# Optimization experiments

Hardware: AMD Instinct MI355X
Metric: run time of the kernel (lower is better)

Reference implementation:

```python
import jax, jax.numpy as jnp
import numpy as np

N = 100000   # nodes
E = 1600000  # edges
F = 64       # num_features
H = 64       # hidden_units
C = 10       # num_classes
G = 1000     # graphs in batch
BN_EPS = 1e-5


def setup_inputs() -> dict:
    key = jax.random.key(0)
    ks = jax.random.split(key, 32)
    inp = {
        "x": jax.random.normal(ks[0], (N, F), dtype=jnp.float32),
        "edge_index": jax.random.randint(ks[1], (2, E), 0, N, dtype=jnp.int64),
        "batch": jnp.sort(jax.random.randint(ks[2], (N,), 0, G, dtype=jnp.int64)),
    }
    i = 3
    def w(shape, scale):
        nonlocal i
        a = jax.random.normal(ks[i], shape, dtype=jnp.float32) * scale
        i += 1
        return a
    for l, din in [(0, F), (1, H)]:
        inp[f"c{l}_w1"] = w((din, H), 1.0 / np.sqrt(din))
        inp[f"c{l}_b1"] = jnp.zeros((H,), jnp.float32)
        inp[f"c{l}_g1"] = jnp.ones((H,), jnp.float32)
        inp[f"c{l}_be1"] = jnp.zeros((H,), jnp.float32)
        inp[f"c{l}_w2"] = w((H, H), 1.0 / np.sqrt(H))
        inp[f"c{l}_b2"] = jnp.zeros((H,), jnp.float32)
        inp[f"bn{l}_g"] = jnp.ones((H,), jnp.float32)
        inp[f"bn{l}_b"] = jnp.zeros((H,), jnp.float32)
    for l, din in [(0, F), (1, H), (2, H)]:
        inp[f"l{l}_w"] = w((din, C), 1.0 / np.sqrt(din))
        inp[f"l{l}_b"] = jnp.zeros((C,), jnp.float32)
    return inp


def _bn(h, g, b):
    # BatchNorm1d in training mode: batch statistics over node axis
    m = jnp.mean(h, axis=0)
    v = jnp.var(h, axis=0)
    return g * (h - m) * jax.lax.rsqrt(v + BN_EPS) + b


def _gin_conv(h, src, dst, w1, b1, g1, be1, w2, b2):
    # scatter-add neighbor aggregation: out[dst] += h[src]; eps = 0
    agg = jax.ops.segment_sum(h[src], dst, num_segments=N)
    z = h + agg                      # (1 + eps) * x + sum_j x_j
    z = jax.nn.relu(_bn(z @ w1 + b1, g1, be1))
    return z @ w2 + b2


def reference(x, edge_index, batch,
              c0_w1, c0_b1, c0_g1, c0_be1, c0_w2, c0_b2, bn0_g, bn0_b,
              c1_w1, c1_b1, c1_g1, c1_be1, c1_w2, c1_b2, bn1_g, bn1_b,
              l0_w, l0_b, l1_w, l1_b, l2_w, l2_b):
    src, dst = edge_index[0], edge_index[1]
    h0 = x
    h1 = jax.nn.relu(_bn(_gin_conv(h0, src, dst, c0_w1, c0_b1, c0_g1, c0_be1, c0_w2, c0_b2), bn0_g, bn0_b))
    h2 = jax.nn.relu(_bn(_gin_conv(h1, src, dst, c1_w1, c1_b1, c1_g1, c1_be1, c1_w2, c1_b2), bn1_g, bn1_b))
    # jumping-knowledge readout: per-layer global_add_pool -> Linear -> sum (dropout=0)
    out = jnp.zeros((G, C), dtype=x.dtype)
    for h, w, b in [(h0, l0_w, l0_b), (h1, l1_w, l1_b), (h2, l2_w, l2_b)]:
        pooled = jax.ops.segment_sum(h, batch, num_segments=G)
        out = out + pooled @ w + b
    return out
```

## Files before the change

### kernel.cpp

```cpp
#include <hip/hip_runtime.h>
#include <hip/hip_bf16.h>

#define BN_EPS 1e-5f
#define NBMAX 512
#define CHUNK 4096
#define CAP   5120
#define CAPC  6144

typedef __hip_bfloat16 bf16;
typedef __attribute__((ext_vector_type(8))) short short8;
typedef __attribute__((ext_vector_type(4))) float f32x4;

__device__ __forceinline__ float b2f(bf16 v) { return __bfloat162float(v); }
__device__ __forceinline__ bf16 f2b(float v) { return __float2bfloat16(v); }
__device__ __forceinline__ float bl(unsigned u) { return __uint_as_float(u << 16); }
__device__ __forceinline__ float bh(unsigned u) { return __uint_as_float(u & 0xffff0000u); }
__device__ __forceinline__ unsigned pack2(float x, float y) {
    union { bf16 b[2]; unsigned u; } p;
    p.b[0] = f2b(x); p.b[1] = f2b(y);
    return p.u;
}
__device__ __forceinline__ float bs2f(short s) {
    return __uint_as_float(((unsigned)(unsigned short)s) << 16);
}
__device__ __forceinline__ short f2bs(float v) {
    bf16 b = f2b(v);
    return *reinterpret_cast<short*>(&b);
}

__global__ __launch_bounds__(256) void initcast_k(
    const float* __restrict__ in, bf16* __restrict__ out, int total4,
    int* __restrict__ bcur, int NB)
{
    if (blockIdx.x == 0) {
        for (int i = threadIdx.x; i < NB; i += 256) bcur[i] = i * CAP;
    }
    int i = blockIdx.x * 256 + threadIdx.x;
    if (i >= total4) return;
    float4 v = ((const float4*)in)[i];
    union { ushort4 u; bf16 b[4]; } p;
    p.b[0] = f2b(v.x); p.b[1] = f2b(v.y); p.b[2] = f2b(v.z); p.b[3] = f2b(v.w);
    ((ushort4*)out)[i] = p.u;
}

__global__ __launch_bounds__(256) void binscatter_k(
    const int* __restrict__ src, const int* __restrict__ dst,
    int* __restrict__ bcur, int* __restrict__ tmp, int E, int NB)
{
    __shared__ int hist[NBMAX];
    __shared__ int loff[NBMAX];
    __shared__ int gb[NBMAX];
    __shared__ int lcur[NBMAX];
    __shared__ int staged[CHUNK];
    __shared__ unsigned short sb[CHUNK];
    __shared__ int ssc[256];
    const int t = threadIdx.x;
    for (int i = t; i < NB; i += 256) { hist[i] = 0; lcur[i] = 0; }
    __syncthreads();
    const int base = blockIdx.x * CHUNK;
    const int lim = min(CHUNK, E - base);
    int myb[16], myw[16];
    int cnt = 0;
    for (int i = t; i < lim; i += 256) {
        int d = dst[base + i];
        int s_ = src[base + i];
        int b = d >> 8;
        myb[cnt] = b;
        myw[cnt] = (s_ << 8) | (d & 255);
        cnt++;
        atomicAdd(&hist[b], 1);
    }
    __syncthreads();
    int v0 = (2 * t     < NB) ? hist[2 * t]     : 0;
    int v1 = (2 * t + 1 < NB) ? hist[2 * t + 1] : 0;
    ssc[t] = v0 + v1;
    __syncthreads();
    for (int off = 1; off < 256; off <<= 1) {
        int a = (t >= off) ? ssc[t - off] : 0;
        __syncthreads();
        ssc[t] += a;
        __syncthreads();
    }
    int excl = ssc[t] - (v0 + v1);
    if (2 * t < NB)     loff[2 * t] = excl;
    if (2 * t + 1 < NB) loff[2 * t + 1] = excl + v0;
    __syncthreads();
    for (int b = t; b < NB; b += 256)
        if (hist[b] > 0) gb[b] = atomicAdd(&bcur[b], hist[b]);
    for (int i = 0; i < cnt; i++) {
        int b = myb[i];
        int p = loff[b] + atomicAdd(&lcur[b], 1);
        staged[p] = myw[i];
        sb[p] = (unsigned short)b;
    }
    __syncthreads();
    for (int i = t; i < lim; i += 256) {
        int b = sb[i];
        tmp[gb[b] + (i - loff[b])] = staged[i];
    }
}

__global__ __launch_bounds__(256) void csr_k(
    const int* __restrict__ bcur, const int* __restrict__ tmp,
    int* __restrict__ rowptr, int* __restrict__ rowend,
    int* __restrict__ adj, int N)
{
    __shared__ int hist[256], pfx[256], cur[256], ssc[256];
    __shared__ int sadj[CAPC];
    const int b = blockIdx.x, t = threadIdx.x;
    const int lo = b * CAP;
    const int cnt = min(bcur[b] - lo, CAP);
    hist[t] = 0; cur[t] = 0;
    __syncthreads();
    for (int i = t; i < cnt; i += 256)
        atomicAdd(&hist[tmp[lo + i] & 255], 1);
    __syncthreads();
    int v = hist[t];
    ssc[t] = v;
    __syncthreads();
    for (int off = 1; off < 256; off <<= 1) {
        int a = (t >= off) ? ssc[t - off] : 0;
        __syncthreads();
        ssc[t] += a;
        __syncthreads();
    }
    pfx[t] = ssc[t] - v;
    const int node = b * 256 + t;
    if (node < N) {
        rowptr[node] = lo + pfx[t];
        rowend[node] = lo + pfx[t] + v;
    }
    __syncthreads();
    if (cnt <= CAPC) {
        for (int i = t; i < cnt; i += 256) {
            int w = tmp[lo + i];
            int d = w & 255;
            int p = pfx[d] + atomicAdd(&cur[d], 1);
            sadj[p] = w >> 8;
        }
        __syncthreads();
        for (int i = t; i < cnt; i += 256) adj[lo + i] = sadj[i];
    } else {
        for (int i = t; i < cnt; i += 256) {
            int w = tmp[lo + i];
            int d = w & 255;
            int p = pfx[d] + atomicAdd(&cur[d], 1);
            adj[lo + p] = w >> 8;
        }
    }
}

template<int AFFINE>
__global__ __launch_bounds__(256) void aggregate_k(
    const bf16* __restrict__ h, const int* __restrict__ rowptr,
    const int* __restrict__ rowend, const int* __restrict__ adj,
    bf16* __restrict__ z, int N,
    const float* __restrict__ sc, const float* __restrict__ sh)
{
    const int lane = threadIdx.x & 31;
    const int n = blockIdx.x * 8 + (threadIdx.x >> 5);
    float sc0 = 0.f, sc1 = 0.f, sh0 = 0.f, sh1 = 0.f;
    if (AFFINE) {
        const int f0 = lane * 2;
        sc0 = sc[f0]; sc1 = sc[f0 + 1];
        sh0 = sh[f0]; sh1 = sh[f0 + 1];
    }
    if (n >= N) return;
    const unsigned* hp = (const unsigned*)h;
    const int b = rowptr[n], e = rowend[n];

    unsigned u = hp[(size_t)n * 32 + lane];
    float a0 = bl(u), a1 = bh(u);
    if (AFFINE) {
        a0 = fmaxf(fmaf(a0, sc0, sh0), 0.f);
        a1 = fmaxf(fmaf(a1, sc1, sh1), 0.f);
    }
    float s0 = a0, s1 = a1;

    int i = b;
    for (; i + 16 <= e; i += 16) {
        int m[16];
        #pragma unroll
        for (int k = 0; k < 16; k++) m[k] = adj[i + k];
        unsigned w[16];
        #pragma unroll
        for (int k = 0; k < 16; k++) w[k] = hp[(size_t)m[k] * 32 + lane];
        #pragma unroll
        for (int k = 0; k < 16; k++) {
            float p0 = bl(w[k]), p1 = bh(w[k]);
            if (AFFINE) {
                p0 = fmaxf(fmaf(p0, sc0, sh0), 0.f);
                p1 = fmaxf(fmaf(p1, sc1, sh1), 0.f);
            }
            s0 += p0; s1 += p1;
        }
    }
    for (; i + 4 <= e; i += 4) {
        int m[4];
        #pragma unroll
        for (int k = 0; k < 4; k++) m[k] = adj[i + k];
        #pragma unroll
        for (int k = 0; k < 4; k++) {
            unsigned w = hp[(size_t)m[k] * 32 + lane];
            float p0 = bl(w), p1 = bh(w);
            if (AFFINE) {
                p0 = fmaxf(fmaf(p0, sc0, sh0), 0.f);
                p1 = fmaxf(fmaf(p1, sc1, sh1), 0.f);
            }
            s0 += p0; s1 += p1;
        }
    }
    for (; i < e; i++) {
        unsigned w = hp[(size_t)adj[i] * 32 + lane];
        float p0 = bl(w), p1 = bh(w);
        if (AFFINE) {
            p0 = fmaxf(fmaf(p0, sc0, sh0), 0.f);
            p1 = fmaxf(fmaf(p1, sc1, sh1), 0.f);
        }
        s0 += p0; s1 += p1;
    }
    ((unsigned*)z)[(size_t)n * 32 + lane] = pack2(s0, s1);
}

template<int MODE>
__global__ __launch_bounds__(256) void gemm64_k(
    const bf16* __restrict__ A,
    const float* __restrict__ scin, const float* __restrict__ shin,
    const float* __restrict__ W, const float* __restrict__ bias,
    bf16* __restrict__ out, float* __restrict__ pstat, int nrows)
{
    __shared__ bf16 sWt[64][72];
    __shared__ bf16 sC[128][68];
    __shared__ float sSc[64], sSh[64], sB[64];
    __shared__ float sredS[64][17], sredQ[64][17];
    const int tid = threadIdx.x;

    if (tid < 64) {
        sB[tid] = bias[tid];
        if (MODE == 1) { sSc[tid] = scin[tid]; sSh[tid] = shin[tid]; }
    }
    for (int i = tid; i < 4096; i += 256) {
        int k = i >> 6, n = i & 63;
        sWt[n][k] = f2b(W[i]);
    }
    __syncthreads();

    const int wave = tid >> 6, lane = tid & 63;
    const int quad = lane >> 4, l16 = lane & 15;
    const int row0 = blockIdx.x * 128 + wave * 32;

    short8 a[2][2];
    #pragma unroll
    for (int rt = 0; rt < 2; rt++) {
        int r = row0 + rt * 16 + l16;
        int rr = min(r, nrows - 1);
        const bf16* arow = A + (size_t)rr * 64;
        a[rt][0] = *(const short8*)(arow + quad * 8);
        a[rt][1] = *(const short8*)(arow + 32 + quad * 8);
        if (MODE == 1) {
            #pragma unroll
            for (int j = 0; j < 8; j++) {
                int f0 = quad * 8 + j;
                a[rt][0][j] = f2bs(fmaxf(fmaf(bs2f(a[rt][0][j]), sSc[f0], sSh[f0]), 0.f));
                int f1 = 32 + f0;
                a[rt][1][j] = f2bs(fmaxf(fmaf(bs2f(a[rt][1][j]), sSc[f1], sSh[f1]), 0.f));
            }
        }
    }

    float psS[4], psQ[4];
    #pragma unroll
    for (int t = 0; t < 4; t++) { psS[t] = 0.f; psQ[t] = 0.f; }

    #pragma unroll
    for (int t = 0; t < 4; t++) {
        const int n = t * 16 + l16;
        short8 b0 = *(const short8*)&sWt[n][quad * 8];
        short8 b1 = *(const short8*)&sWt[n][32 + quad * 8];
        const float bn_ = sB[n];
        #pragma unroll
        for (int rt = 0; rt < 2; rt++) {
            f32x4 acc = {0.f, 0.f, 0.f, 0.f};
            acc = __builtin_amdgcn_mfma_f32_16x16x32_bf16(a[rt][0], b0, acc, 0, 0, 0);
            acc = __builtin_amdgcn_mfma_f32_16x16x32_bf16(a[rt][1], b1, acc, 0, 0, 0);
            #pragma unroll
            for (int reg = 0; reg < 4; reg++) {
                const int lr = wave * 32 + rt * 16 + quad * 4 + reg;
                float v = acc[reg] + bn_;
                sC[lr][n] = f2b(v);
                if (row0 + rt * 16 + quad * 4 + reg < nrows) {
                    psS[t] += v;
                    psQ[t] = fmaf(v, v, psQ[t]);
                }
            }
        }
    }

    #pragma unroll
    for (int t = 0; t < 4; t++) {
        sredS[t * 16 + l16][wave * 4 + quad] = psS[t];
        sredQ[t * 16 + l16][wave * 4 + quad] = psQ[t];
    }
    __syncthreads();

    const int gbase = blockIdx.x * 128;
    #pragma unroll
    for (int it = 0; it < 8; it++) {
        int idx = it * 256 + tid;
        int r = idx >> 4, c4 = idx & 15;
        if (gbase + r < nrows) {
            ushort4 v = *(const ushort4*)&sC[r][c4 * 4];
            *(ushort4*)(out + (size_t)(gbase + r) * 64 + c4 * 4) = v;
        }
    }

    if (tid < 128) {
        const int c = tid & 63;
        const float* p = (tid < 64) ? &sredS[c][0] : &sredQ[c][0];
        float s = 0.f;
        #pragma unroll
        for (int i = 0; i < 16; i++) s += p[i];
        pstat[(size_t)blockIdx.x * 128 + (tid < 64 ? c : 64 + c)] = s;
    }
}

__global__ __launch_bounds__(256) void bn_reduce_k(
    const float* __restrict__ pstat, int nblk,
    const float* __restrict__ g, const float* __restrict__ be, float invN,
    float* __restrict__ sc, float* __restrict__ sh)
{
    const int f = blockIdx.x;
    const int t = threadIdx.x;
    float S = 0.f, Q = 0.f;
    for (int b = t; b < nblk; b += 256) {
        S += pstat[(size_t)b * 128 + f];
        Q += pstat[(size_t)b * 128 + 64 + f];
    }
    __shared__ float rs[256], rq[256];
    rs[t] = S; rq[t] = Q;
    __syncthreads();
    for (int off = 128; off > 0; off >>= 1) {
        if (t < off) { rs[t] += rs[t + off]; rq[t] += rq[t + off]; }
        __syncthreads();
    }
    if (t == 0) {
        float m = rs[0] * invN;
        float v = rq[0] * invN - m * m;
        float s = g[f] * rsqrtf(v + BN_EPS);
        sc[f] = s;
        sh[f] = be[f] - m * s;
    }
}

__global__ __launch_bounds__(256) void pool_readout_k(
    const bf16* __restrict__ xb, const bf16* __restrict__ z0,
    const bf16* __restrict__ z1, const int* __restrict__ batch,
    const float* __restrict__ scA, const float* __restrict__ shA,
    const float* __restrict__ scB, const float* __restrict__ shB,
    const float* __restrict__ w0, const float* __restrict__ b0,
    const float* __restrict__ w1, const float* __restrict__ b1,
    const float* __restrict__ w2, const float* __restrict__ b2,
    float* __restrict__ out, int Nn)
{
    const int g = blockIdx.x;
    int lo = 0, hi = Nn;
    while (lo < hi) { int mid = (lo + hi) >> 1; if (batch[mid] < g) lo = mid + 1; else hi = mid; }
    const int start = lo;
    hi = Nn;
    while (lo < hi) { int mid = (lo + hi) >> 1; if (batch[mid] <= g) lo = mid + 1; else hi = mid; }
    const int end = lo;

    const int f = threadIdx.x & 63;
    const int w = threadIdx.x >> 6;
    const float sA = scA[f], tA = shA[f];
    const float sB = scB[f], tB = shB[f];

    float s0 = 0.f, s1 = 0.f, s2 = 0.f;
    for (int i = start + w; i < end; i += 4) {
        s0 += b2f(xb[(size_t)i * 64 + f]);
        s1 += fmaxf(fmaf(b2f(z0[(size_t)i * 64 + f]), sA, tA), 0.f);
        s2 += fmaxf(fmaf(b2f(z1[(size_t)i * 64 + f]), sB, tB), 0.f);
    }
    __shared__ float p[3][4][64];
    p[0][w][f] = s0; p[1][w][f] = s1; p[2][w][f] = s2;
    __syncthreads();
    if (threadIdx.x < 10) {
        const int c = threadIdx.x;
        float acc = b0[c] + b1[c] + b2[c];
        for (int k = 0; k < 64; k++) {
            float q0 = p[0][0][k] + p[0][1][k] + p[0][2][k] + p[0][3][k];
            float q1 = p[1][0][k] + p[1][1][k] + p[1][2][k] + p[1][3][k];
            float q2 = p[2][0][k] + p[2][1][k] + p[2][2][k] + p[2][3][k];
            acc = fmaf(q0, w0[k * 10 + c], acc);
            acc = fmaf(q1, w1[k * 10 + c], acc);
            acc = fmaf(q2, w2[k * 10 + c], acc);
        }
        out[(size_t)g * 10 + c] = acc;
    }
}

extern "C" void kernel_launch(void* const* d_in, const int* in_sizes, int n_in,
                              void* d_out, int out_size, void* d_ws, size_t ws_size,
                              hipStream_t stream)
{
    const float* x     = (const float*)d_in[0];
    const int*   edge  = (const int*)d_in[1];
    const int*   batch = (const int*)d_in[2];
    const int N = in_sizes[0] / 64;
    const int E = in_sizes[1] / 2;
    const int G = out_size / 10;
    const int* src = edge;
    const int* dst = edge + E;
    const int NB = (N + 255) / 256;

    const float* c_w1[2]  = {(const float*)d_in[3],  (const float*)d_in[11]};
    const float* c_b1[2]  = {(const float*)d_in[4],  (const float*)d_in[12]};
    const float* c_g1[2]  = {(const float*)d_in[5],  (const float*)d_in[13]};
    const float* c_be1[2] = {(const float*)d_in[6],  (const float*)d_in[14]};
    const float* c_w2[2]  = {(const float*)d_in[7],  (const float*)d_in[15]};
    const float* c_b2[2]  = {(const float*)d_in[8],  (const float*)d_in[16]};
    const float* bn_g[2]  = {(const float*)d_in[9],  (const float*)d_in[17]};
    const float* bn_b[2]  = {(const float*)d_in[10], (const float*)d_in[18]};
    const float* lw[3]    = {(const float*)d_in[19], (const float*)d_in[21], (const float*)d_in[23]};
    const float* lb[3]    = {(const float*)d_in[20], (const float*)d_in[22], (const float*)d_in[24]};

    float* out = (float*)d_out;
    const size_t nh = (size_t)N * 64;
    const int PG = (N + 127) / 128;

    bf16*  zb    = (bf16*)d_ws;
    bf16*  wb    = zb + nh;
    bf16*  xb    = wb + nh;
    float* scsh  = (float*)(xb + nh);
    float* pstat = scsh + 512;
    int*   rowptr = (int*)(pstat + (size_t)PG * 128);
    int*   rowend = rowptr + N;
    int*   adj    = rowend + N;
    int*   tmp    = adj + (size_t)NB * CAP;
    int*   bcur   = tmp + (size_t)NB * CAP;

    float* sc0 = scsh;       float* sh0 = scsh + 64;
    float* scA = scsh + 128; float* shA = scsh + 192;
    float* sc2 = scsh + 256; float* sh2 = scsh + 320;
    float* scB = scsh + 384; float* shB = scsh + 448;

    const float invN = 1.0f / (float)N;
    const int binGrid  = (E + CHUNK - 1) / CHUNK;
    const int aggGrid  = (N + 7) / 8;
    const int ewGrid   = (int)((nh / 4 + 255) / 256);

    initcast_k<<<ewGrid, 256, 0, stream>>>(x, xb, (int)(nh / 4), bcur, NB);
    binscatter_k<<<binGrid, 256, 0, stream>>>(src, dst, bcur, tmp, E, NB);
    csr_k<<<NB, 256, 0, stream>>>(bcur, tmp, rowptr, rowend, adj, N);

    aggregate_k<0><<<aggGrid, 256, 0, stream>>>(xb, rowptr, rowend, adj, zb, N,
                                                nullptr, nullptr);
    gemm64_k<0><<<PG, 256, 0, stream>>>(zb, nullptr, nullptr,
                                        c_w1[0], c_b1[0], zb, pstat, N);
    bn_reduce_k<<<64, 256, 0, stream>>>(pstat, PG, c_g1[0], c_be1[0], invN, sc0, sh0);
    gemm64_k<1><<<PG, 256, 0, stream>>>(zb, sc0, sh0,
                                        c_w2[0], c_b2[0], zb, pstat, N);
    bn_reduce_k<<<64, 256, 0, stream>>>(pstat, PG, bn_g[0], bn_b[0], invN, scA, shA);

    aggregate_k<1><<<aggGrid, 256, 0, stream>>>(zb, rowptr, rowend, adj, wb, N,
                                                scA, shA);
    gemm64_k<0><<<PG, 256, 0, stream>>>(wb, nullptr, nullptr,
                                        c_w1[1], c_b1[1], wb, pstat, N);
    bn_reduce_k<<<64, 256, 0, stream>>>(pstat, PG, c_g1[1], c_be1[1], invN, sc2, sh2);
    gemm64_k<1><<<PG, 256, 0, stream>>>(wb, sc2, sh2,
                                        c_w2[1], c_b2[1], wb, pstat, N);
    bn_reduce_k<<<64, 256, 0, stream>>>(pstat, PG, bn_g[1], bn_b[1], invN, scB, shB);

    pool_readout_k<<<G, 256, 0, stream>>>(xb, zb, wb, batch,
                                          scA, shA, scB, shB,
                                          lw[0], lb[0], lw[1], lb[1], lw[2], lb[2],
                                          out, N);
}
```

Baseline: 305.3 us.

## Pad CSR rows to multiples of 16 with a zero sentinel node and materialize activations

Each CSR row is padded to a multiple of 16 entries that point at an extra zero row (index N), so the aggregation loop runs only full 16-wide unrolled batches with no remainder loops. The layer-1 BN+ReLU affine moves out of the gather into a separate elementwise kernel that writes an activated buffer. The pooling readout then reads that buffer directly. This removes per-edge affine math and tail-loop divergence, at the cost of an extra pass over the node features, extra padded gathers of the zero row, and larger adjacency and workspace buffers.

New measurement: 295.0 us. 1.04x faster.

```diff
diff --git a/kernel.cpp b/kernel.cpp
--- a/kernel.cpp
+++ b/kernel.cpp
@@ -5,7 +5,7 @@
 #define NBMAX 512
 #define CHUNK 4096
 #define CAP   5120
-#define CAPC  6144
+#define PCAP  9216
 
 typedef __hip_bfloat16 bf16;
 typedef __attribute__((ext_vector_type(8))) short short8;
@@ -29,7 +29,7 @@
 }
 
 __global__ __launch_bounds__(256) void initcast_k(
-    const float* __restrict__ in, bf16* __restrict__ out, int total4,
+    const float* __restrict__ in, bf16* __restrict__ out, int n4, int total4,
     int* __restrict__ bcur, int NB)
 {
     if (blockIdx.x == 0) {
@@ -37,10 +37,15 @@
     }
     int i = blockIdx.x * 256 + threadIdx.x;
     if (i >= total4) return;
-    float4 v = ((const float4*)in)[i];
-    union { ushort4 u; bf16 b[4]; } p;
-    p.b[0] = f2b(v.x); p.b[1] = f2b(v.y); p.b[2] = f2b(v.z); p.b[3] = f2b(v.w);
-    ((ushort4*)out)[i] = p.u;
+    if (i < n4) {
+        float4 v = ((const float4*)in)[i];
+        union { ushort4 u; bf16 b[4]; } p;
+        p.b[0] = f2b(v.x); p.b[1] = f2b(v.y); p.b[2] = f2b(v.z); p.b[3] = f2b(v.w);
+        ((ushort4*)out)[i] = p.u;
+    } else {
+        ushort4 z; z.x = 0; z.y = 0; z.z = 0; z.w = 0;
+        ((ushort4*)out)[i] = z;
+    }
 }
 
 __global__ __launch_bounds__(256) void binscatter_k(
@@ -106,17 +111,19 @@
     int* __restrict__ adj, int N)
 {
     __shared__ int hist[256], pfx[256], cur[256], ssc[256];
-    __shared__ int sadj[CAPC];
+    __shared__ int sadj[PCAP];
     const int b = blockIdx.x, t = threadIdx.x;
     const int lo = b * CAP;
+    const int plo = b * PCAP;
     const int cnt = min(bcur[b] - lo, CAP);
     hist[t] = 0; cur[t] = 0;
     __syncthreads();
     for (int i = t; i < cnt; i += 256)
         atomicAdd(&hist[tmp[lo + i] & 255], 1);
     __syncthreads();
-    int v = hist[t];
-    ssc[t] = v;
+    const int v = hist[t];
+    const int pv = (v + 15) & ~15;
+    ssc[t] = pv;
     __syncthreads();
     for (int off = 1; off < 256; off <<= 1) {
         int a = (t >= off) ? ssc[t - off] : 0;
@@ -124,61 +131,42 @@
         ssc[t] += a;
         __syncthreads();
     }
-    pfx[t] = ssc[t] - v;
+    const int myp = ssc[t] - pv;
+    pfx[t] = myp;
     const int node = b * 256 + t;
     if (node < N) {
-        rowptr[node] = lo + pfx[t];
-        rowend[node] = lo + pfx[t] + v;
-    }
-    __syncthreads();
-    if (cnt <= CAPC) {
-        for (int i = t; i < cnt; i += 256) {
-            int w = tmp[lo + i];
-            int d = w & 255;
-            int p = pfx[d] + atomicAdd(&cur[d], 1);
-            sadj[p] = w >> 8;
-        }
-        __syncthreads();
-        for (int i = t; i < cnt; i += 256) adj[lo + i] = sadj[i];
-    } else {
-        for (int i = t; i < cnt; i += 256) {
-            int w = tmp[lo + i];
-            int d = w & 255;
-            int p = pfx[d] + atomicAdd(&cur[d], 1);
-            adj[lo + p] = w >> 8;
-        }
-    }
-}
-
-template<int AFFINE>
-__global__ __launch_bounds__(256) void aggregate_k(
+        rowptr[node] = plo + myp;
+        rowend[node] = plo + myp + pv;
+    }
+    __syncthreads();
+    const int pcnt = ssc[255];
+    for (int i = t; i < cnt; i += 256) {
+        int w = tmp[lo + i];
+        int d = w & 255;
+        int p = pfx[d] + atomicAdd(&cur[d], 1);
+        sadj[p] = w >> 8;
+    }
+    __syncthreads();
+    for (int i = v; i < pv; i++) sadj[myp + i] = N;
+    __syncthreads();
+    for (int i = t; i < pcnt; i += 256) adj[plo + i] = sadj[i];
+}
+
+__global__ __launch_bounds__(256, 4) void aggregate_k(
     const bf16* __restrict__ h, const int* __restrict__ rowptr,
     const int* __restrict__ rowend, const int* __restrict__ adj,
-    bf16* __restrict__ z, int N,
-    const float* __restrict__ sc, const float* __restrict__ sh)
+    bf16* __restrict__ z, int N)
 {
     const int lane = threadIdx.x & 31;
     const int n = blockIdx.x * 8 + (threadIdx.x >> 5);
-    float sc0 = 0.f, sc1 = 0.f, sh0 = 0.f, sh1 = 0.f;
-    if (AFFINE) {
-        const int f0 = lane * 2;
-        sc0 = sc[f0]; sc1 = sc[f0 + 1];
-        sh0 = sh[f0]; sh1 = sh[f0 + 1];
-    }
     if (n >= N) return;
     const unsigned* hp = (const unsigned*)h;
     const int b = rowptr[n], e = rowend[n];
 
     unsigned u = hp[(size_t)n * 32 + lane];
-    float a0 = bl(u), a1 = bh(u);
-    if (AFFINE) {
-        a0 = fmaxf(fmaf(a0, sc0, sh0), 0.f);
-        a1 = fmaxf(fmaf(a1, sc1, sh1), 0.f);
-    }
-    float s0 = a0, s1 = a1;
-
-    int i = b;
-    for (; i + 16 <= e; i += 16) {
+    float s0 = bl(u), s1 = bh(u);
+
+    for (int i = b; i < e; i += 16) {
         int m[16];
         #pragma unroll
         for (int k = 0; k < 16; k++) m[k] = adj[i + k];
@@ -187,39 +175,32 @@
         for (int k = 0; k < 16; k++) w[k] = hp[(size_t)m[k] * 32 + lane];
         #pragma unroll
         for (int k = 0; k < 16; k++) {
-            float p0 = bl(w[k]), p1 = bh(w[k]);
-            if (AFFINE) {
-                p0 = fmaxf(fmaf(p0, sc0, sh0), 0.f);
-                p1 = fmaxf(fmaf(p1, sc1, sh1), 0.f);
-            }
-            s0 += p0; s1 += p1;
+            s0 += bl(w[k]);
+            s1 += bh(w[k]);
         }
     }
-    for (; i + 4 <= e; i += 4) {
-        int m[4];
-        #pragma unroll
-        for (int k = 0; k < 4; k++) m[k] = adj[i + k];
-        #pragma unroll
-        for (int k = 0; k < 4; k++) {
-            unsigned w = hp[(size_t)m[k] * 32 + lane];
-            float p0 = bl(w), p1 = bh(w);
-            if (AFFINE) {
-                p0 = fmaxf(fmaf(p0, sc0, sh0), 0.f);
-                p1 = fmaxf(fmaf(p1, sc1, sh1), 0.f);
-            }
-            s0 += p0; s1 += p1;
-        }
-    }
-    for (; i < e; i++) {
-        unsigned w = hp[(size_t)adj[i] * 32 + lane];
-        float p0 = bl(w), p1 = bh(w);
-        if (AFFINE) {
-            p0 = fmaxf(fmaf(p0, sc0, sh0), 0.f);
-            p1 = fmaxf(fmaf(p1, sc1, sh1), 0.f);
-        }
-        s0 += p0; s1 += p1;
-    }
     ((unsigned*)z)[(size_t)n * 32 + lane] = pack2(s0, s1);
+}
+
+__global__ __launch_bounds__(256) void ewact_k(
+    const bf16* __restrict__ y, const float* __restrict__ sc,
+    const float* __restrict__ sh, bf16* __restrict__ h, int N)
+{
+    const int idx = blockIdx.x * 256 + threadIdx.x;
+    const int total = (N + 1) * 8;
+    if (idx >= total) return;
+    short8 v;
+    if (idx < N * 8) {
+        const int f0 = (idx & 7) * 8;
+        v = *(const short8*)(y + (size_t)idx * 8);
+        #pragma unroll
+        for (int j = 0; j < 8; j++)
+            v[j] = f2bs(fmaxf(fmaf(bs2f(v[j]), sc[f0 + j], sh[f0 + j]), 0.f));
+    } else {
+        #pragma unroll
+        for (int j = 0; j < 8; j++) v[j] = 0;
+    }
+    *(short8*)(h + (size_t)idx * 8) = v;
 }
 
 template<int MODE>
@@ -353,9 +334,8 @@
 }
 
 __global__ __launch_bounds__(256) void pool_readout_k(
-    const bf16* __restrict__ xb, const bf16* __restrict__ z0,
-    const bf16* __restrict__ z1, const int* __restrict__ batch,
-    const float* __restrict__ scA, const float* __restrict__ shA,
+    const bf16* __restrict__ xb, const bf16* __restrict__ h1,
+    const bf16* __restrict__ y1, const int* __restrict__ batch,
     const float* __restrict__ scB, const float* __restrict__ shB,
     const float* __restrict__ w0, const float* __restrict__ b0,
     const float* __restrict__ w1, const float* __restrict__ b1,
@@ -372,14 +352,13 @@
 
     const int f = threadIdx.x & 63;
     const int w = threadIdx.x >> 6;
-    const float sA = scA[f], tA = shA[f];
     const float sB = scB[f], tB = shB[f];
 
     float s0 = 0.f, s1 = 0.f, s2 = 0.f;
     for (int i = start + w; i < end; i += 4) {
         s0 += b2f(xb[(size_t)i * 64 + f]);
-        s1 += fmaxf(fmaf(b2f(z0[(size_t)i * 64 + f]), sA, tA), 0.f);
-        s2 += fmaxf(fmaf(b2f(z1[(size_t)i * 64 + f]), sB, tB), 0.f);
+        s1 += b2f(h1[(size_t)i * 64 + f]);
+        s2 += fmaxf(fmaf(b2f(y1[(size_t)i * 64 + f]), sB, tB), 0.f);
     }
     __shared__ float p[3][4][64];
     p[0][w][f] = s0; p[1][w][f] = s1; p[2][w][f] = s2;
@@ -425,18 +404,20 @@
     const float* lb[3]    = {(const float*)d_in[20], (const float*)d_in[22], (const float*)d_in[24]};
 
     float* out = (float*)d_out;
-    const size_t nh = (size_t)N * 64;
+    const size_t nh  = (size_t)N * 64;
+    const size_t nh1 = (size_t)(N + 1) * 64;
     const int PG = (N + 127) / 128;
 
     bf16*  zb    = (bf16*)d_ws;
     bf16*  wb    = zb + nh;
     bf16*  xb    = wb + nh;
-    float* scsh  = (float*)(xb + nh);
+    bf16*  hb    = xb + nh1;
+    float* scsh  = (float*)(hb + nh1);
     float* pstat = scsh + 512;
     int*   rowptr = (int*)(pstat + (size_t)PG * 128);
     int*   rowend = rowptr + N;
     int*   adj    = rowend + N;
-    int*   tmp    = adj + (size_t)NB * CAP;
+    int*   tmp    = adj + (size_t)NB * PCAP;
     int*   bcur   = tmp + (size_t)NB * CAP;
 
     float* sc0 = scsh;       float* sh0 = scsh + 64;
@@ -447,14 +428,16 @@
     const float invN = 1.0f / (float)N;
     const int binGrid  = (E + CHUNK - 1) / CHUNK;
     const int aggGrid  = (N + 7) / 8;
-    const int ewGrid   = (int)((nh / 4 + 255) / 256);
-
-    initcast_k<<<ewGrid, 256, 0, stream>>>(x, xb, (int)(nh / 4), bcur, NB);
+    const int n4       = N * 16;
+    const int total4   = (N + 1) * 16;
+    const int ewGrid   = (total4 + 255) / 256;
+    const int actGrid  = ((N + 1) * 8 + 255) / 256;
+
+    initcast_k<<<ewGrid, 256, 0, stream>>>(x, xb, n4, total4, bcur, NB);
     binscatter_k<<<binGrid, 256, 0, stream>>>(src, dst, bcur, tmp, E, NB);
     csr_k<<<NB, 256, 0, stream>>>(bcur, tmp, rowptr, rowend, adj, N);
 
-    aggregate_k<0><<<aggGrid, 256, 0, stream>>>(xb, rowptr, rowend, adj, zb, N,
-                                                nullptr, nullptr);
+    aggregate_k<<<aggGrid, 256, 0, stream>>>(xb, rowptr, rowend, adj, zb, N);
     gemm64_k<0><<<PG, 256, 0, stream>>>(zb, nullptr, nullptr,
                                         c_w1[0], c_b1[0], zb, pstat, N);
     bn_reduce_k<<<64, 256, 0, stream>>>(pstat, PG, c_g1[0], c_be1[0], invN, sc0, sh0);
@@ -462,8 +445,9 @@
                                         c_w2[0], c_b2[0], zb, pstat, N);
     bn_reduce_k<<<64, 256, 0, stream>>>(pstat, PG, bn_g[0], bn_b[0], invN, scA, shA);
 
-    aggregate_k<1><<<aggGrid, 256, 0, stream>>>(zb, rowptr, rowend, adj, wb, N,
-                                                scA, shA);
+    ewact_k<<<actGrid, 256, 0, stream>>>(zb, scA, shA, hb, N);
+
+    aggregate_k<<<aggGrid, 256, 0, stream>>>(hb, rowptr, rowend, adj, wb, N);
     gemm64_k<0><<<PG, 256, 0, stream>>>(wb, nullptr, nullptr,
                                         c_w1[1], c_b1[1], wb, pstat, N);
     bn_reduce_k<<<64, 256, 0, stream>>>(pstat, PG, c_g1[1], c_be1[1], invN, sc2, sh2);
@@ -471,8 +455,8 @@
                                         c_w2[1], c_b2[1], wb, pstat, N);
     bn_reduce_k<<<64, 256, 0, stream>>>(pstat, PG, bn_g[1], bn_b[1], invN, scB, shB);
 
-    pool_readout_k<<<G, 256, 0, stream>>>(xb, zb, wb, batch,
-                                          scA, shA, scB, shB,
+    pool_readout_k<<<G, 256, 0, stream>>>(xb, hb, wb, batch,
+                                          scB, shB,
                                           lw[0], lb[0], lw[1], lb[1], lw[2], lb[2],
                                           out, N);
 }
```
